# Performance work log

Hardware: AMD Instinct MI355X
Metric: run time of the kernel (lower is better)

Reference implementation:

```python
import jax, jax.numpy as jnp
import numpy as np

N = 100000   # neurons
R = 4        # receptor types (tau_syns has 4 entries)
E = 2000000  # synapses
T = 50       # timesteps
B = 1        # batch
DT = 1.0
DAMP = 0.3      # dampening_factor for pseudo-derivative
REC_DAMP = 0.5  # recurrent_dampening_factor


@jax.custom_vjp
def spike_function(v_scaled, dampening_factor):
    return (v_scaled > 0.0).astype(v_scaled.dtype)


def _spike_fwd(v_scaled, dampening_factor):
    return spike_function(v_scaled, dampening_factor), (v_scaled, dampening_factor)


def _spike_bwd(res, g):
    v_scaled, d = res
    dz_dv = d * jnp.maximum(1.0 - jnp.abs(v_scaled), 0.0)  # pseudo_derivative
    return (g * dz_dv, jnp.zeros_like(d))


spike_function.defvjp(_spike_fwd, _spike_bwd)


def setup_inputs() -> dict:
    key = jax.random.key(0)
    ks = jax.random.split(key, 11)
    tau_syns = jnp.array([5.5, 8.5, 2.8, 5.8], jnp.float32)
    return {
        "w_rec": jax.random.normal(ks[0], (E,), jnp.float32) * 0.01,
        "x_ext": jax.random.normal(ks[1], (T, B, N * R), jnp.float32) * 0.05,
        "v0": jax.random.uniform(ks[2], (B, N), jnp.float32),
        "v_th": jnp.ones((N,), jnp.float32),           # normalized threshold
        "v_reset": jnp.zeros((N,), jnp.float32),       # normalized reset
        "t_ref": jnp.full((N,), 2.0, jnp.float32),
        "decay": jax.random.uniform(ks[3], (N,), jnp.float32, minval=0.8, maxval=0.99),
        "current_factor": jax.random.uniform(ks[4], (N,), jnp.float32, minval=0.5, maxval=1.5),
        "e_l_current": jax.random.normal(ks[5], (N,), jnp.float32) * 0.01,
        "asc_amps": jax.random.normal(ks[6], (N, 2), jnp.float32) * 0.01,
        "asc_decay": jax.random.uniform(ks[7], (N, 2), jnp.float32, minval=0.7, maxval=0.99),
        "syn_decay": jnp.exp(-DT / tau_syns),
        "psc_init": jnp.float32(np.e) / tau_syns,
        "pre_idx": jax.random.randint(ks[8], (E,), 0, N, jnp.int32),
        "post_idx": jax.random.randint(ks[9], (E,), 0, N, jnp.int32),
        "receptor_idx": jax.random.randint(ks[10], (E,), 0, R, jnp.int32),
    }


def reference(w_rec, x_ext, v0, v_th, v_reset, t_ref, decay, current_factor,
              e_l_current, asc_amps, asc_decay, syn_decay, psc_init,
              pre_idx, post_idx, receptor_idx):
    # flat (neuron, receptor) slot layout: slot = neuron*R + receptor
    seg_ids = post_idx * R + receptor_idx
    syn_d = jnp.tile(syn_decay, N)[None, :]   # [1, N*R]
    psc_i = jnp.tile(psc_init, N)[None, :]    # [1, N*R]
    damp = jnp.float32(DAMP)

    def step(carry, x_t):
        z, v, r, asc, psc, psc_rise = carry
        # gradient dampening on recurrent spikes (same forward value as z)
        rec_z = REC_DAMP * z + (1.0 - REC_DAMP) * jax.lax.stop_gradient(z)
        # sparse gather-multiply-scatter: [B,E] -> [B, N*R]
        contrib = rec_z[:, pre_idx] * w_rec[None, :]
        rec_in = jax.vmap(
            lambda c: jax.ops.segment_sum(c, seg_ids, num_segments=N * R)
        )(contrib)
        inputs = rec_in + x_t
        # double-exponential synaptic filtering
        new_psc_rise = psc_rise * syn_d + inputs * psc_i
        new_psc = psc * syn_d + DT * syn_d * psc_rise
        # after-spike currents (2 channels)
        new_asc = asc_decay[None] * asc + z[..., None] * asc_amps[None]
        input_current = new_psc.reshape(B, N, R).sum(-1) + asc.sum(-1)  # [B,N]
        # soft reset from previous spike
        reset_current = z * (v_reset - v_th)[None]
        new_v = decay[None] * v + current_factor[None] * (input_current + e_l_current[None]) + reset_current
        # normalized voltage (E_L normalized to 0, so normalizer = v_th)
        v_sc = (new_v - v_th[None]) / v_th[None]
        new_z = spike_function(v_sc, damp)
        new_z = jnp.where(r > 0.0, jnp.zeros_like(new_z), new_z)  # refractory
        new_r = jnp.maximum(r - DT + new_z * t_ref[None], 0.0)
        return (new_z, new_v, new_r, new_asc, new_psc, new_psc_rise), new_z

    carry0 = (
        jnp.zeros((B, N), jnp.float32),      # z
        v0,                                  # v
        jnp.zeros((B, N), jnp.float32),      # refractory counter
        jnp.zeros((B, N, 2), jnp.float32),   # asc
        jnp.zeros((B, N * R), jnp.float32),  # psc
        jnp.zeros((B, N * R), jnp.float32),  # psc_rise
    )
    _, spikes = jax.lax.scan(step, carry0, x_ext)
    return spikes  # [T, B, N]
```

## Files before the change

kernel.cpp:

```cpp
#include <hip/hip_runtime.h>


constexpr int RR  = 4;
constexpr int BS  = 1024;
constexpr int BKN = 512;
constexpr int NCH = 512;

__global__ void count_kernel(const int* __restrict__ post, int* __restrict__ ghist,
                             unsigned long long* __restrict__ mA,
                             unsigned long long* __restrict__ mB,
                             unsigned* __restrict__ barr,
                             int E, int CH, int NBK, int nmask, int nbar) {
    __shared__ int h[256];
    for (int i = threadIdx.x; i < NBK; i += blockDim.x) h[i] = 0;
    __syncthreads();
    const int b = blockIdx.x, lo = b * CH, hi = min(lo + CH, E);
    for (int e = lo + threadIdx.x; e < hi; e += blockDim.x)
        atomicAdd(&h[post[e] >> 9], 1);
    __syncthreads();
    for (int i = threadIdx.x; i < NBK; i += blockDim.x)
        ghist[i * NCH + b] = h[i];
    int g = blockIdx.x * blockDim.x + threadIdx.x;
    int gs = gridDim.x * blockDim.x;
    for (int i = g; i < nmask; i += gs) { mA[i] = 0ull; mB[i] = 0ull; }
    for (int i = g; i < nbar; i += gs) barr[i] = 0u;
}

__global__ void scanA_kernel(int* __restrict__ ghist, int* __restrict__ rtot,
                             int* __restrict__ ptot) {
    __shared__ int s[NCH];
    const int i = blockIdx.x, tid = threadIdx.x;
    int v = ghist[i * NCH + tid];
    s[tid] = v;
    __syncthreads();
    for (int off = 1; off < NCH; off <<= 1) {
        int t = (tid >= off) ? s[tid - off] : 0;
        __syncthreads();
        s[tid] += t;
        __syncthreads();
    }
    ghist[i * NCH + tid] = s[tid] - v;
    if (tid == NCH - 1) {
        int tot = s[tid];
        rtot[i] = tot;
        ptot[i] = (tot + 3) & ~3;
    }
}

__global__ void scanB_kernel(const int* __restrict__ rtot, const int* __restrict__ ptot,
                             int* __restrict__ bstart,
                             unsigned* __restrict__ epack, float* __restrict__ ew,
                             int NBK) {
    __shared__ int s[256];
    const int tid = threadIdx.x;
    int v = (tid < NBK) ? ptot[tid] : 0;
    s[tid] = v;
    __syncthreads();
    for (int off = 1; off < 256; off <<= 1) {
        int t = (tid >= off) ? s[tid - off] : 0;
        __syncthreads();
        s[tid] += t;
        __syncthreads();
    }
    if (tid < NBK) bstart[tid] = s[tid] - v;
    if (tid == NBK - 1) bstart[NBK] = s[tid];
    __syncthreads();
    if (tid < NBK) {
        int base = bstart[tid];
        for (int k = base + rtot[tid]; k < base + ptot[tid]; ++k) {
            epack[k] = 0u; ew[k] = 0.f;
        }
    }
}

__global__ void fill_kernel(const int* __restrict__ pre, const int* __restrict__ post,
                            const int* __restrict__ rc, const float* __restrict__ w,
                            const int* __restrict__ ghist, const int* __restrict__ bstart,
                            unsigned* __restrict__ epack, float* __restrict__ ew,
                            int E, int CH, int NBK) {
    __shared__ int cur[256];
    const int b = blockIdx.x;
    for (int i = threadIdx.x; i < NBK; i += blockDim.x)
        cur[i] = bstart[i] + ghist[i * NCH + b];
    __syncthreads();
    const int lo = b * CH, hi = min(lo + CH, E);
    for (int e = lo + threadIdx.x; e < hi; e += blockDim.x) {
        int pn = post[e];
        int k = atomicAdd(&cur[pn >> 9], 1);
        epack[k] = (unsigned)pre[e] | ((unsigned)rc[e] << 18)
                 | ((unsigned)(pn & (BKN - 1)) << 20);
        ew[k] = w[e];
    }
}

__device__ __forceinline__ void test4(const uint4 pk, const float4 wv,
                                      const unsigned long long* smask,
                                      float* sacc) {
    unsigned a = pk.x & 0x3FFFFu, b = pk.y & 0x3FFFFu;
    unsigned c = pk.z & 0x3FFFFu, d = pk.w & 0x3FFFFu;
    if ((smask[a >> 6] >> (a & 63)) & 1ull) atomicAdd(&sacc[pk.x >> 18], wv.x);
    if ((smask[b >> 6] >> (b & 63)) & 1ull) atomicAdd(&sacc[pk.y >> 18], wv.y);
    if ((smask[c >> 6] >> (c & 63)) & 1ull) atomicAdd(&sacc[pk.z >> 18], wv.z);
    if ((smask[d >> 6] >> (d & 63)) & 1ull) atomicAdd(&sacc[pk.w >> 18], wv.w);
}

__global__ void __launch_bounds__(BS, 4)
sim_kernel(const float4* __restrict__ x_ext4,
           const float* __restrict__ v0,  const float* __restrict__ v_th,
           const float* __restrict__ v_rst, const float* __restrict__ t_rf,
           const float* __restrict__ decay, const float* __restrict__ curf,
           const float* __restrict__ e_l,
           const float2* __restrict__ aamps, const float2* __restrict__ adec,
           const float* __restrict__ syn_d4, const float* __restrict__ psc_i4,
           const uint4* __restrict__ epack4, const float4* __restrict__ ew4,
           const int* __restrict__ bstart,
           unsigned long long* __restrict__ mA, unsigned long long* __restrict__ mB,
           unsigned* __restrict__ barr,
           float* __restrict__ out, int N, int nmask, int T)
{
    extern __shared__ unsigned long long sdyn[];
    unsigned long long* smask = sdyn;
    float* sacc = (float*)(sdyn + nmask);
    const int tid = threadIdx.x;
    const int n = blockIdx.x * BKN + tid;
    const bool own = (tid < BKN) && (n < N);
    const unsigned nblk = gridDim.x;

    float psc0 = 0.f, psc1 = 0.f, psc2 = 0.f, psc3 = 0.f;
    float pr0 = 0.f, pr1 = 0.f, pr2 = 0.f, pr3 = 0.f;
    float vv = 0.f, rr_ = 0.f, zz = 0.f, a0 = 0.f, a1 = 0.f;
    float vth = 1.f, dvr = 0.f, trf = 0.f, dec = 0.f, cf = 0.f, el = 0.f;
    float aa0 = 0.f, aa1 = 0.f, ad0 = 0.f, ad1 = 0.f;
    if (own) {
        vv  = v0[n];
        vth = v_th[n];  dvr = v_rst[n] - vth;
        trf = t_rf[n];  dec = decay[n];
        cf  = curf[n];  el  = e_l[n];
        float2 aa = aamps[n]; aa0 = aa.x; aa1 = aa.y;
        float2 ad = adec[n];  ad0 = ad.x; ad1 = ad.y;
    }
    const float sd0 = syn_d4[0], sd1 = syn_d4[1], sd2 = syn_d4[2], sd3 = syn_d4[3];
    const float pi0 = psc_i4[0], pi1 = psc_i4[1], pi2 = psc_i4[2], pi3 = psc_i4[3];

    const int q_lo = bstart[blockIdx.x] >> 2;
    const int q_hi = bstart[blockIdx.x + 1] >> 2;
    const int i0 = q_lo + tid, i1 = i0 + BS, i2 = i1 + BS, i3 = i2 + BS;
    const uint4 z4 = make_uint4(0u, 0u, 0u, 0u);
    const float4 zf = make_float4(0.f, 0.f, 0.f, 0.f);
    uint4  qa = (i0 < q_hi) ? epack4[i0] : z4;
    uint4  qb = (i1 < q_hi) ? epack4[i1] : z4;
    uint4  qc = (i2 < q_hi) ? epack4[i2] : z4;
    uint4  qd = (i3 < q_hi) ? epack4[i3] : z4;
    float4 wa = (i0 < q_hi) ? ew4[i0] : zf;
    float4 wb = (i1 < q_hi) ? ew4[i1] : zf;
    float4 wc = (i2 < q_hi) ? ew4[i2] : zf;
    float4 wd = (i3 < q_hi) ? ew4[i3] : zf;
    const bool overflow = (q_hi - q_lo) > 4 * BS;

    const int g = blockIdx.x & 7;
    const unsigned gsize = (nblk - (unsigned)g + 7u) >> 3;

    for (int i = tid; i < nmask; i += BS) smask[i] = 0ull;
    sacc[tid] = 0.f; sacc[tid + BS] = 0.f;
    float4 xt = own ? x_ext4[n] : zf;
    int anyspk = 0;
    __syncthreads();

    for (int t = 0; t < T; ++t) {
        float nz = 0.f;
        float npc0, npc1, npc2, npc3;
        if (own) {
            npc0 = psc0 * sd0 + sd0 * pr0;
            npc1 = psc1 * sd1 + sd1 * pr1;
            npc2 = psc2 * sd2 + sd2 * pr2;
            npc3 = psc3 * sd3 + sd3 * pr3;
            float in_cur = npc0 + npc1 + npc2 + npc3;
            float asum = a0 + a1;
            float nv = dec * vv + cf * (in_cur + asum + el) + zz * dvr;
            nz = (nv > vth) ? 1.f : 0.f;
            if (rr_ > 0.f) nz = 0.f;
            rr_ = fmaxf(rr_ - 1.f + nz * trf, 0.f);
            a0 = ad0 * a0 + zz * aa0;
            a1 = ad1 * a1 + zz * aa1;
            psc0 = npc0; psc1 = npc1; psc2 = npc2; psc3 = npc3;
            vv = nv;
        }
        const bool lastT = (t + 1 >= T);

        unsigned long long bal = __ballot(nz > 0.f);
        if (!lastT) {
            unsigned long long* gmo = (t & 1) ? mB : mA;
            if (own && (tid & 63) == 0)
                __hip_atomic_store(&gmo[n >> 6], bal, __ATOMIC_RELAXED,
                                   __HIP_MEMORY_SCOPE_AGENT);
            asm volatile("s_waitcnt vmcnt(0)" ::: "memory");
        }
        __syncthreads();

        bool i_released = false;
        if (!lastT && tid == 0) {
            unsigned* bg  = barr + (size_t)t * 160 + (size_t)g * 16;
            unsigned* btp = barr + (size_t)t * 160 + 128;
            unsigned* rl  = barr + (size_t)t * 160 + 144;
            unsigned old = __hip_atomic_fetch_add(bg, 1u, __ATOMIC_RELAXED,
                                                  __HIP_MEMORY_SCOPE_AGENT);
            if (old == gsize - 1u) {
                unsigned ot = __hip_atomic_fetch_add(btp, 1u, __ATOMIC_RELAXED,
                                                     __HIP_MEMORY_SCOPE_AGENT);
                if (ot == 7u) {
                    __hip_atomic_store(rl, 1u, __ATOMIC_RELAXED,
                                       __HIP_MEMORY_SCOPE_AGENT);
                    i_released = true;
                }
            }
        }

        if (anyspk) {
            test4(qa, wa, smask, sacc);
            test4(qb, wb, smask, sacc);
            test4(qc, wc, smask, sacc);
            test4(qd, wd, smask, sacc);
            if (overflow) {
                for (int q = q_lo + tid + 4 * BS; q < q_hi; q += BS)
                    test4(epack4[q], ew4[q], smask, sacc);
            }
        }
        __syncthreads();

        if (own) {
            float acc0 = sacc[tid * 4 + 0], acc1 = sacc[tid * 4 + 1];
            float acc2 = sacc[tid * 4 + 2], acc3 = sacc[tid * 4 + 3];
            sacc[tid * 4 + 0] = 0.f; sacc[tid * 4 + 1] = 0.f;
            sacc[tid * 4 + 2] = 0.f; sacc[tid * 4 + 3] = 0.f;
            pr0 = pr0 * sd0 + (acc0 + xt.x) * pi0;
            pr1 = pr1 * sd1 + (acc1 + xt.y) * pi1;
            pr2 = pr2 * sd2 + (acc2 + xt.z) * pi2;
            pr3 = pr3 * sd3 + (acc3 + xt.w) * pi3;
            out[(size_t)t * N + n] = nz;
            zz = nz;
        }

        if (!lastT) {
            float4 xtn = own ? x_ext4[(size_t)(t + 1) * N + n] : zf;

            if (tid == 0 && !i_released) {
                unsigned* rl = barr + (size_t)t * 160 + 144;
                while (!__hip_atomic_load(rl, __ATOMIC_RELAXED,
                                          __HIP_MEMORY_SCOPE_AGENT))
                    __builtin_amdgcn_s_sleep(1);
            }
            __syncthreads();

            const unsigned long long* gm = (t & 1) ? mB : mA;
            unsigned long long m0 = 0ull, m1 = 0ull;
            if (tid < nmask)
                m0 = __hip_atomic_load(&gm[tid], __ATOMIC_RELAXED,
                                       __HIP_MEMORY_SCOPE_AGENT);
            if (tid + BS < nmask)
                m1 = __hip_atomic_load(&gm[tid + BS], __ATOMIC_RELAXED,
                                       __HIP_MEMORY_SCOPE_AGENT);
            if (tid < nmask) smask[tid] = m0;
            if (tid + BS < nmask) smask[tid + BS] = m1;
            anyspk = __syncthreads_or((m0 | m1) != 0ull ? 1 : 0);
            xt = xtn;
        }
    }
}

extern "C" void kernel_launch(void* const* d_in, const int* in_sizes, int n_in,
                              void* d_out, int out_size, void* d_ws, size_t ws_size,
                              hipStream_t stream) {
    const float* w_rec = (const float*)d_in[0];
    const float* x_ext = (const float*)d_in[1];
    const float* v0    = (const float*)d_in[2];
    const float* v_th  = (const float*)d_in[3];
    const float* v_rst = (const float*)d_in[4];
    const float* t_rf  = (const float*)d_in[5];
    const float* decay = (const float*)d_in[6];
    const float* curf  = (const float*)d_in[7];
    const float* e_l   = (const float*)d_in[8];
    const float* aamps = (const float*)d_in[9];
    const float* adec  = (const float*)d_in[10];
    const float* syn_d = (const float*)d_in[11];
    const float* psc_i = (const float*)d_in[12];
    const int*   pre   = (const int*)d_in[13];
    const int*   post  = (const int*)d_in[14];
    const int*   rc    = (const int*)d_in[15];

    const int E = in_sizes[0];
    const int N = in_sizes[2];
    const int T = in_sizes[1] / (N * RR);
    const int nmask = (N + 63) / 64;
    const int NBK = (N + BKN - 1) / BKN;
    const int CH  = (E + NCH - 1) / NCH;
    const int nbar = 160 * T;
    const int EP  = E + 4 * NBK;

    char* ws = (char*)d_ws;
    unsigned* epack  = (unsigned*)ws;                     ws += (size_t)EP * 4;
    float*    ew     = (float*)ws;                        ws += (size_t)EP * 4;
    unsigned long long* maskA = (unsigned long long*)ws;  ws += (size_t)nmask * 8;
    unsigned long long* maskB = (unsigned long long*)ws;  ws += (size_t)nmask * 8;
    int* ghist       = (int*)ws;                          ws += (size_t)NBK * NCH * 4;
    int* rtot        = (int*)ws;                          ws += (size_t)NBK * 4;
    int* ptot        = (int*)ws;                          ws += (size_t)NBK * 4;
    int* bstart      = (int*)ws;                          ws += (size_t)(NBK + 1) * 4;
    unsigned* barr   = (unsigned*)ws;

    count_kernel<<<NCH, 256, 0, stream>>>(post, ghist, maskA, maskB, barr,
                                          E, CH, NBK, nmask, nbar);
    scanA_kernel<<<NBK, NCH, 0, stream>>>(ghist, rtot, ptot);
    scanB_kernel<<<1, 256, 0, stream>>>(rtot, ptot, bstart, epack, ew, NBK);
    fill_kernel<<<NCH, 256, 0, stream>>>(pre, post, rc, w_rec, ghist, bstart,
                                         epack, ew, E, CH, NBK);

    const size_t smbytes = (size_t)nmask * 8 + (size_t)BKN * RR * 4;
    sim_kernel<<<NBK, BS, smbytes, stream>>>(
        (const float4*)x_ext, v0, v_th, v_rst, t_rf, decay, curf, e_l,
        (const float2*)aamps, (const float2*)adec, syn_d, psc_i,
        (const uint4*)epack, (const float4*)ew, bstart, maskA, maskB, barr,
        (float*)d_out, N, nmask, T);
}
```

Measured before the change: 483.1 us.

## Replace hierarchical atomic grid barrier with per-block flag polling and 4-deep mask ring

Swaps the two-level atomic-counter grid barrier for per-block monotonically increasing step flags. At each step one wavefront polls all block flags until they reach the current step. Spike masks move from double buffering to a 4-slot ring, so slowing blocks cannot have their mask overwritten before peers read it. The wait is now placed before the synapse accumulation instead of after it. This removes atomic contention on shared counters and the serialized release chain, at the cost of every block polling about 196 flags per step.

```diff
diff --git a/kernel.cpp b/kernel.cpp
--- a/kernel.cpp
+++ b/kernel.cpp
@@ -7,10 +7,9 @@
 constexpr int NCH = 512;
 
 __global__ void count_kernel(const int* __restrict__ post, int* __restrict__ ghist,
-                             unsigned long long* __restrict__ mA,
-                             unsigned long long* __restrict__ mB,
-                             unsigned* __restrict__ barr,
-                             int E, int CH, int NBK, int nmask, int nbar) {
+                             unsigned long long* __restrict__ msk,
+                             unsigned* __restrict__ flags,
+                             int E, int CH, int NBK, int nmask4) {
     __shared__ int h[256];
     for (int i = threadIdx.x; i < NBK; i += blockDim.x) h[i] = 0;
     __syncthreads();
@@ -22,8 +21,8 @@
         ghist[i * NCH + b] = h[i];
     int g = blockIdx.x * blockDim.x + threadIdx.x;
     int gs = gridDim.x * blockDim.x;
-    for (int i = g; i < nmask; i += gs) { mA[i] = 0ull; mB[i] = 0ull; }
-    for (int i = g; i < nbar; i += gs) barr[i] = 0u;
+    for (int i = g; i < nmask4; i += gs) msk[i] = 0ull;
+    for (int i = g; i < NBK; i += gs) flags[i] = 0u;
 }
 
 __global__ void scanA_kernel(int* __restrict__ ghist, int* __restrict__ rtot,
@@ -114,8 +113,8 @@
            const float* __restrict__ syn_d4, const float* __restrict__ psc_i4,
            const uint4* __restrict__ epack4, const float4* __restrict__ ew4,
            const int* __restrict__ bstart,
-           unsigned long long* __restrict__ mA, unsigned long long* __restrict__ mB,
-           unsigned* __restrict__ barr,
+           unsigned long long* __restrict__ msk,
+           unsigned* __restrict__ flags,
            float* __restrict__ out, int N, int nmask, int T)
 {
     extern __shared__ unsigned long long sdyn[];
@@ -124,7 +123,7 @@
     const int tid = threadIdx.x;
     const int n = blockIdx.x * BKN + tid;
     const bool own = (tid < BKN) && (n < N);
-    const unsigned nblk = gridDim.x;
+    const int nblk = (int)gridDim.x;
 
     float psc0 = 0.f, psc1 = 0.f, psc2 = 0.f, psc3 = 0.f;
     float pr0 = 0.f, pr1 = 0.f, pr2 = 0.f, pr3 = 0.f;
@@ -157,23 +156,20 @@
     float4 wd = (i3 < q_hi) ? ew4[i3] : zf;
     const bool overflow = (q_hi - q_lo) > 4 * BS;
 
-    const int g = blockIdx.x & 7;
-    const unsigned gsize = (nblk - (unsigned)g + 7u) >> 3;
-
     for (int i = tid; i < nmask; i += BS) smask[i] = 0ull;
     sacc[tid] = 0.f; sacc[tid + BS] = 0.f;
     float4 xt = own ? x_ext4[n] : zf;
-    int anyspk = 0;
     __syncthreads();
 
     for (int t = 0; t < T; ++t) {
+        const bool lastT = (t + 1 >= T);
+
         float nz = 0.f;
-        float npc0, npc1, npc2, npc3;
         if (own) {
-            npc0 = psc0 * sd0 + sd0 * pr0;
-            npc1 = psc1 * sd1 + sd1 * pr1;
-            npc2 = psc2 * sd2 + sd2 * pr2;
-            npc3 = psc3 * sd3 + sd3 * pr3;
+            float npc0 = psc0 * sd0 + sd0 * pr0;
+            float npc1 = psc1 * sd1 + sd1 * pr1;
+            float npc2 = psc2 * sd2 + sd2 * pr2;
+            float npc3 = psc3 * sd3 + sd3 * pr3;
             float in_cur = npc0 + npc1 + npc2 + npc3;
             float asum = a0 + a1;
             float nv = dec * vv + cf * (in_cur + asum + el) + zz * dvr;
@@ -185,34 +181,56 @@
             psc0 = npc0; psc1 = npc1; psc2 = npc2; psc3 = npc3;
             vv = nv;
         }
-        const bool lastT = (t + 1 >= T);
 
         unsigned long long bal = __ballot(nz > 0.f);
         if (!lastT) {
-            unsigned long long* gmo = (t & 1) ? mB : mA;
             if (own && (tid & 63) == 0)
-                __hip_atomic_store(&gmo[n >> 6], bal, __ATOMIC_RELAXED,
-                                   __HIP_MEMORY_SCOPE_AGENT);
+                __hip_atomic_store(&msk[(size_t)(t & 3) * nmask + (n >> 6)], bal,
+                                   __ATOMIC_RELAXED, __HIP_MEMORY_SCOPE_AGENT);
             asm volatile("s_waitcnt vmcnt(0)" ::: "memory");
         }
         __syncthreads();
 
-        bool i_released = false;
-        if (!lastT && tid == 0) {
-            unsigned* bg  = barr + (size_t)t * 160 + (size_t)g * 16;
-            unsigned* btp = barr + (size_t)t * 160 + 128;
-            unsigned* rl  = barr + (size_t)t * 160 + 144;
-            unsigned old = __hip_atomic_fetch_add(bg, 1u, __ATOMIC_RELAXED,
-                                                  __HIP_MEMORY_SCOPE_AGENT);
-            if (old == gsize - 1u) {
-                unsigned ot = __hip_atomic_fetch_add(btp, 1u, __ATOMIC_RELAXED,
-                                                     __HIP_MEMORY_SCOPE_AGENT);
-                if (ot == 7u) {
-                    __hip_atomic_store(rl, 1u, __ATOMIC_RELAXED,
-                                       __HIP_MEMORY_SCOPE_AGENT);
-                    i_released = true;
+        if (!lastT && tid == 0)
+            __hip_atomic_store(&flags[blockIdx.x], (unsigned)(t + 1),
+                               __ATOMIC_RELAXED, __HIP_MEMORY_SCOPE_AGENT);
+
+        int anyspk = 0;
+        if (t > 0) {
+            if (tid < 64) {
+                const unsigned target = (unsigned)t;
+                for (;;) {
+                    unsigned f0 = (tid < nblk)
+                        ? __hip_atomic_load(&flags[tid], __ATOMIC_RELAXED,
+                                            __HIP_MEMORY_SCOPE_AGENT) : target;
+                    unsigned f1 = (tid + 64 < nblk)
+                        ? __hip_atomic_load(&flags[tid + 64], __ATOMIC_RELAXED,
+                                            __HIP_MEMORY_SCOPE_AGENT) : target;
+                    unsigned f2 = (tid + 128 < nblk)
+                        ? __hip_atomic_load(&flags[tid + 128], __ATOMIC_RELAXED,
+                                            __HIP_MEMORY_SCOPE_AGENT) : target;
+                    unsigned f3 = (tid + 192 < nblk)
+                        ? __hip_atomic_load(&flags[tid + 192], __ATOMIC_RELAXED,
+                                            __HIP_MEMORY_SCOPE_AGENT) : target;
+                    bool bad = (f0 < target) | (f1 < target) |
+                               (f2 < target) | (f3 < target);
+                    if (__ballot(bad) == 0ull) break;
+                    __builtin_amdgcn_s_sleep(1);
                 }
             }
+            __syncthreads();
+
+            const unsigned long long* gm = msk + (size_t)((t - 1) & 3) * nmask;
+            unsigned long long m0 = 0ull, m1 = 0ull;
+            if (tid < nmask)
+                m0 = __hip_atomic_load(&gm[tid], __ATOMIC_RELAXED,
+                                       __HIP_MEMORY_SCOPE_AGENT);
+            if (tid + BS < nmask)
+                m1 = __hip_atomic_load(&gm[tid + BS], __ATOMIC_RELAXED,
+                                       __HIP_MEMORY_SCOPE_AGENT);
+            if (tid < nmask) smask[tid] = m0;
+            if (tid + BS < nmask) smask[tid + BS] = m1;
+            anyspk = __syncthreads_or((m0 | m1) != 0ull ? 1 : 0);
         }
 
         if (anyspk) {
@@ -239,31 +257,8 @@
             out[(size_t)t * N + n] = nz;
             zz = nz;
         }
-
-        if (!lastT) {
-            float4 xtn = own ? x_ext4[(size_t)(t + 1) * N + n] : zf;
-
-            if (tid == 0 && !i_released) {
-                unsigned* rl = barr + (size_t)t * 160 + 144;
-                while (!__hip_atomic_load(rl, __ATOMIC_RELAXED,
-                                          __HIP_MEMORY_SCOPE_AGENT))
-                    __builtin_amdgcn_s_sleep(1);
-            }
-            __syncthreads();
-
-            const unsigned long long* gm = (t & 1) ? mB : mA;
-            unsigned long long m0 = 0ull, m1 = 0ull;
-            if (tid < nmask)
-                m0 = __hip_atomic_load(&gm[tid], __ATOMIC_RELAXED,
-                                       __HIP_MEMORY_SCOPE_AGENT);
-            if (tid + BS < nmask)
-                m1 = __hip_atomic_load(&gm[tid + BS], __ATOMIC_RELAXED,
-                                       __HIP_MEMORY_SCOPE_AGENT);
-            if (tid < nmask) smask[tid] = m0;
-            if (tid + BS < nmask) smask[tid + BS] = m1;
-            anyspk = __syncthreads_or((m0 | m1) != 0ull ? 1 : 0);
-            xt = xtn;
-        }
+        if (!lastT)
+            xt = own ? x_ext4[(size_t)(t + 1) * N + n] : zf;
     }
 }
 
@@ -293,22 +288,20 @@
     const int nmask = (N + 63) / 64;
     const int NBK = (N + BKN - 1) / BKN;
     const int CH  = (E + NCH - 1) / NCH;
-    const int nbar = 160 * T;
     const int EP  = E + 4 * NBK;
 
     char* ws = (char*)d_ws;
     unsigned* epack  = (unsigned*)ws;                     ws += (size_t)EP * 4;
     float*    ew     = (float*)ws;                        ws += (size_t)EP * 4;
-    unsigned long long* maskA = (unsigned long long*)ws;  ws += (size_t)nmask * 8;
-    unsigned long long* maskB = (unsigned long long*)ws;  ws += (size_t)nmask * 8;
+    unsigned long long* msk = (unsigned long long*)ws;    ws += (size_t)4 * nmask * 8;
     int* ghist       = (int*)ws;                          ws += (size_t)NBK * NCH * 4;
     int* rtot        = (int*)ws;                          ws += (size_t)NBK * 4;
     int* ptot        = (int*)ws;                          ws += (size_t)NBK * 4;
     int* bstart      = (int*)ws;                          ws += (size_t)(NBK + 1) * 4;
-    unsigned* barr   = (unsigned*)ws;
-
-    count_kernel<<<NCH, 256, 0, stream>>>(post, ghist, maskA, maskB, barr,
-                                          E, CH, NBK, nmask, nbar);
+    unsigned* flags  = (unsigned*)ws;
+
+    count_kernel<<<NCH, 256, 0, stream>>>(post, ghist, msk, flags,
+                                          E, CH, NBK, 4 * nmask);
     scanA_kernel<<<NBK, NCH, 0, stream>>>(ghist, rtot, ptot);
     scanB_kernel<<<1, 256, 0, stream>>>(rtot, ptot, bstart, epack, ew, NBK);
     fill_kernel<<<NCH, 256, 0, stream>>>(pre, post, rc, w_rec, ghist, bstart,
@@ -318,6 +311,6 @@
     sim_kernel<<<NBK, BS, smbytes, stream>>>(
         (const float4*)x_ext, v0, v_th, v_rst, t_rf, decay, curf, e_l,
         (const float2*)aamps, (const float2*)adec, syn_d, psc_i,
-        (const uint4*)epack, (const float4*)ew, bstart, maskA, maskB, barr,
+        (const uint4*)epack, (const float4*)ew, bstart, msk, flags,
         (float*)d_out, N, nmask, T);
 }
```

Result: slower. 588.9 us (+21.9%).

## Double neurons per block and keep six edge quads per thread in registers

Applied to the files above, without the earlier changes.

Each block now owns 1024 neurons instead of 512, so every thread owns a neuron and the grid has about half as many blocks. The per-block edge cache grows from 4 to 6 register-resident uint4/float4 pairs per thread, and the shared accumulator is zeroed over 4·BS entries. The aim is fewer participants in the per-timestep grid barrier and full use of each block's threads. The cost is roughly half as many CUs in use, twice the per-block edge-scatter work, and more VGPR pressure under the same launch bounds.

```diff
diff --git a/kernel.cpp b/kernel.cpp
--- a/kernel.cpp
+++ b/kernel.cpp
@@ -3,8 +3,10 @@
 
 constexpr int RR  = 4;
 constexpr int BS  = 1024;
-constexpr int BKN = 512;
+constexpr int BKN = 1024;
+constexpr int BSH = 10;
 constexpr int NCH = 512;
+constexpr int NQ  = 6;
 
 __global__ void count_kernel(const int* __restrict__ post, int* __restrict__ ghist,
                              unsigned long long* __restrict__ mA,
@@ -16,7 +18,7 @@
     __syncthreads();
     const int b = blockIdx.x, lo = b * CH, hi = min(lo + CH, E);
     for (int e = lo + threadIdx.x; e < hi; e += blockDim.x)
-        atomicAdd(&h[post[e] >> 9], 1);
+        atomicAdd(&h[post[e] >> BSH], 1);
     __syncthreads();
     for (int i = threadIdx.x; i < NBK; i += blockDim.x)
         ghist[i * NCH + b] = h[i];
@@ -86,7 +88,7 @@
     const int lo = b * CH, hi = min(lo + CH, E);
     for (int e = lo + threadIdx.x; e < hi; e += blockDim.x) {
         int pn = post[e];
-        int k = atomicAdd(&cur[pn >> 9], 1);
+        int k = atomicAdd(&cur[pn >> BSH], 1);
         epack[k] = (unsigned)pre[e] | ((unsigned)rc[e] << 18)
                  | ((unsigned)(pn & (BKN - 1)) << 20);
         ew[k] = w[e];
@@ -123,7 +125,7 @@
     float* sacc = (float*)(sdyn + nmask);
     const int tid = threadIdx.x;
     const int n = blockIdx.x * BKN + tid;
-    const bool own = (tid < BKN) && (n < N);
+    const bool own = n < N;
     const unsigned nblk = gridDim.x;
 
     float psc0 = 0.f, psc1 = 0.f, psc2 = 0.f, psc3 = 0.f;
@@ -144,36 +146,34 @@
 
     const int q_lo = bstart[blockIdx.x] >> 2;
     const int q_hi = bstart[blockIdx.x + 1] >> 2;
-    const int i0 = q_lo + tid, i1 = i0 + BS, i2 = i1 + BS, i3 = i2 + BS;
     const uint4 z4 = make_uint4(0u, 0u, 0u, 0u);
     const float4 zf = make_float4(0.f, 0.f, 0.f, 0.f);
-    uint4  qa = (i0 < q_hi) ? epack4[i0] : z4;
-    uint4  qb = (i1 < q_hi) ? epack4[i1] : z4;
-    uint4  qc = (i2 < q_hi) ? epack4[i2] : z4;
-    uint4  qd = (i3 < q_hi) ? epack4[i3] : z4;
-    float4 wa = (i0 < q_hi) ? ew4[i0] : zf;
-    float4 wb = (i1 < q_hi) ? ew4[i1] : zf;
-    float4 wc = (i2 < q_hi) ? ew4[i2] : zf;
-    float4 wd = (i3 < q_hi) ? ew4[i3] : zf;
-    const bool overflow = (q_hi - q_lo) > 4 * BS;
+    uint4 q[NQ]; float4 w[NQ];
+#pragma unroll
+    for (int k = 0; k < NQ; ++k) {
+        int idx = q_lo + tid + k * BS;
+        q[k] = (idx < q_hi) ? epack4[idx] : z4;
+        w[k] = (idx < q_hi) ? ew4[idx] : zf;
+    }
+    const bool overflow = (q_hi - q_lo) > NQ * BS;
 
     const int g = blockIdx.x & 7;
     const unsigned gsize = (nblk - (unsigned)g + 7u) >> 3;
 
     for (int i = tid; i < nmask; i += BS) smask[i] = 0ull;
-    sacc[tid] = 0.f; sacc[tid + BS] = 0.f;
+#pragma unroll
+    for (int j = 0; j < RR; ++j) sacc[tid + j * BS] = 0.f;
     float4 xt = own ? x_ext4[n] : zf;
     int anyspk = 0;
     __syncthreads();
 
     for (int t = 0; t < T; ++t) {
         float nz = 0.f;
-        float npc0, npc1, npc2, npc3;
         if (own) {
-            npc0 = psc0 * sd0 + sd0 * pr0;
-            npc1 = psc1 * sd1 + sd1 * pr1;
-            npc2 = psc2 * sd2 + sd2 * pr2;
-            npc3 = psc3 * sd3 + sd3 * pr3;
+            float npc0 = psc0 * sd0 + sd0 * pr0;
+            float npc1 = psc1 * sd1 + sd1 * pr1;
+            float npc2 = psc2 * sd2 + sd2 * pr2;
+            float npc3 = psc3 * sd3 + sd3 * pr3;
             float in_cur = npc0 + npc1 + npc2 + npc3;
             float asum = a0 + a1;
             float nv = dec * vv + cf * (in_cur + asum + el) + zz * dvr;
@@ -216,13 +216,11 @@
         }
 
         if (anyspk) {
-            test4(qa, wa, smask, sacc);
-            test4(qb, wb, smask, sacc);
-            test4(qc, wc, smask, sacc);
-            test4(qd, wd, smask, sacc);
+#pragma unroll
+            for (int k = 0; k < NQ; ++k) test4(q[k], w[k], smask, sacc);
             if (overflow) {
-                for (int q = q_lo + tid + 4 * BS; q < q_hi; q += BS)
-                    test4(epack4[q], ew4[q], smask, sacc);
+                for (int qq = q_lo + tid + NQ * BS; qq < q_hi; qq += BS)
+                    test4(epack4[qq], ew4[qq], smask, sacc);
             }
         }
         __syncthreads();
```

Result: slower. 635.5 us (+31.5%).
